# Performance work log

Hardware: AMD Instinct MI355X
Metric: run time of the kernel (lower is better)

## Reference

```python
import jax, jax.numpy as jnp
import numpy as np

N, M, K, D = 65536, 131072, 8, 64
TAU = 0.3
EPS = 1e-6

def setup_inputs() -> dict:
    key = jax.random.key(0)
    ks = jax.random.split(key, 16)
    s = 0.05
    return {
        "f_pts": jax.random.normal(ks[0], (N, D), jnp.float32),
        "pts": jax.random.uniform(ks[1], (N, 3), jnp.float32) * 10.0,
        "z_latent": jax.random.normal(ks[2], (M, D), jnp.float32) * 0.1,
        "centers": jax.random.uniform(ks[3], (M, 3), jnp.float32) * 10.0,
        "cand_idx": jax.random.randint(ks[4], (N, K), 0, M),
        "sim_w1": jax.random.normal(ks[5], (2 * D + 3, 64), jnp.float32) * s,
        "sim_b1": jnp.zeros((64,), jnp.float32),
        "sim_w2": jax.random.normal(ks[6], (64, 1), jnp.float32) * s,
        "sim_b2": jnp.zeros((1,), jnp.float32),
        "gate_w1": jax.random.normal(ks[7], (2 * D, D), jnp.float32) * s,
        "gate_b1": jnp.zeros((D,), jnp.float32),
        "gate_w2": jax.random.normal(ks[8], (D, 1), jnp.float32) * s,
        "gate_b2": jnp.zeros((1,), jnp.float32),
        "W_ih": jax.random.normal(ks[9], (3 * D, D), jnp.float32) * s,
        "W_hh": jax.random.normal(ks[10], (3 * D, D), jnp.float32) * s,
        "b_ih": jnp.zeros((3 * D,), jnp.float32),
        "b_hh": jnp.zeros((3 * D,), jnp.float32),
    }

def _forward(f_pts, pts, z_latent, centers, sim_w1, sim_b1, sim_w2, sim_b2,
             gate_w1, gate_b1, gate_w2, gate_b2, W_ih, W_hh, b_ih, b_hh, cand_idx):
    n, k = cand_idx.shape
    m, d = z_latent.shape
    # --- gather voxel latents / centers for each (point, candidate) pair ---
    z_c = z_latent[cand_idx]                         # (N,K,D)
    delta = pts[:, None, :] - centers[cand_idx]      # (N,K,3)
    f_b = jnp.broadcast_to(f_pts[:, None, :], (n, k, d))
    # --- similarity MLP ---
    x = jnp.concatenate([f_b, z_c, delta], axis=-1)  # (N,K,2D+3)
    h = jax.nn.relu(x @ sim_w1 + sim_b1)
    sim = (h @ sim_w2 + sim_b2)[..., 0]              # (N,K)
    # --- low-temperature top-K routing weights over candidates ---
    w = jax.nn.softmax(sim / TAU, axis=-1)           # (N,K)
    # --- scatter weighted point features to voxels ---
    flat_idx = cand_idx.reshape(-1)                  # (N*K,)
    contrib = (w[..., None] * f_pts[:, None, :]).reshape(-1, d)
    msg = jax.ops.segment_sum(contrib, flat_idx, num_segments=m)     # (M,D)
    wsum = jax.ops.segment_sum(w.reshape(-1), flat_idx, num_segments=m)
    msg = msg / (wsum[:, None] + EPS)                # normalized voxel message
    # --- per-voxel gate ---
    g_in = jnp.concatenate([z_latent, msg], axis=-1)
    gate = jax.nn.sigmoid(jax.nn.relu(g_in @ gate_w1 + gate_b1) @ gate_w2 + gate_b2)  # (M,1)
    # --- GRUCell (torch layout: rows ordered r,z,n) ---
    gi = msg @ W_ih.T + b_ih
    gh = z_latent @ W_hh.T + b_hh
    i_r, i_z, i_n = jnp.split(gi, 3, axis=-1)
    h_r, h_z, h_n = jnp.split(gh, 3, axis=-1)
    r = jax.nn.sigmoid(i_r + h_r)
    zg = jax.nn.sigmoid(i_z + h_z)
    nn_ = jnp.tanh(i_n + r * h_n)
    h_new = (1.0 - zg) * nn_ + zg * z_latent
    # gated latent update
    return z_latent + gate * (h_new - z_latent)

def reference(f_pts, pts, z_latent, centers, cand_idx, sim_w1, sim_b1, sim_w2, sim_b2,
              gate_w1, gate_b1, gate_w2, gate_b2, W_ih, W_hh, b_ih, b_hh):
    return _forward(f_pts, pts, z_latent, centers, sim_w1, sim_b1, sim_w2, sim_b2,
                    gate_w1, gate_b1, gate_w2, gate_b2, W_ih, W_hh, b_ih, b_hh, cand_idx)
```

## Files before the change

kernel.cpp:

```cpp
#include <hip/hip_runtime.h>
#include <hip/hip_fp16.h>
#include <math.h>


typedef short bf16x8 __attribute__((ext_vector_type(8)));
typedef unsigned short u16x8 __attribute__((ext_vector_type(8)));
typedef float f32x4 __attribute__((ext_vector_type(4)));
#define MFMA __builtin_amdgcn_mfma_f32_16x16x32_bf16
#define CAP 32

__device__ __forceinline__ short f2bf(float f) {
  unsigned u = __float_as_uint(f);
  unsigned r = (u + 0x7FFFu + ((u >> 16) & 1u)) >> 16;
  return (short)r;
}

__device__ __forceinline__ float bf2f(unsigned short h) {
  return __uint_as_float(((unsigned)h) << 16);
}

__device__ __forceinline__ float sigm(float x) { return 1.0f / (1.0f + __expf(-x)); }

__global__ __launch_bounds__(256) void prep0_kernel(
    const float* __restrict__ sim_w1, const float* __restrict__ gate_w1,
    const float* __restrict__ W_ih, const float* __restrict__ W_hh,
    short* __restrict__ bfF, short* __restrict__ bfZC,
    short* __restrict__ GF, short* __restrict__ WihF, short* __restrict__ WhhF,
    int* __restrict__ cursor, int M)
{
  int tid = blockIdx.x * 256 + threadIdx.x;
  int n4 = M >> 2;
  int stride = gridDim.x * 256;
  int4* cp = (int4*)cursor;
  for (int j = tid; j < n4; j += stride) cp[j] = make_int4(0, 0, 0, 0);

  int w = blockIdx.x * 4 + (threadIdx.x >> 6);
  int lane = threadIdx.x & 63, lr = lane & 15, lg = lane >> 4;
  bf16x8 o;

  if (w < 12) {
    int ct = w / 3, kt = w % 3;
#pragma unroll
    for (int e = 0; e < 8; ++e) {
      int k = kt * 32 + lg * 8 + e;
      float v = 0.0f;
      if (kt < 2) v = sim_w1[k * 64 + ct * 16 + lr];
      else if ((k - 64) < 3) v = sim_w1[(128 + (k - 64)) * 64 + ct * 16 + lr];
      o[e] = f2bf(v);
    }
    *(bf16x8*)&bfF[w * 512 + lane * 8] = o;
  } else if (w < 24) {
    int q = w - 12, ct = q / 3, kt = q % 3;
#pragma unroll
    for (int e = 0; e < 8; ++e) {
      int k = kt * 32 + lg * 8 + e;
      float v = 0.0f;
      if (kt < 2) v = sim_w1[(64 + k) * 64 + ct * 16 + lr];
      else if ((k - 64) < 3) v = sim_w1[(128 + (k - 64)) * 64 + ct * 16 + lr];
      o[e] = f2bf(v);
    }
    *(bf16x8*)&bfZC[q * 512 + lane * 8] = o;
  } else if (w < 40) {
    int q = w - 24, ct = q >> 2, kt = q & 3;
#pragma unroll
    for (int e = 0; e < 8; ++e)
      o[e] = f2bf(gate_w1[(kt * 32 + lg * 8 + e) * 64 + ct * 16 + lr]);
    *(bf16x8*)&GF[q * 512 + lane * 8] = o;
  } else if (w < 64) {
    int q = w - 40, g = q >> 3, ct = (q >> 1) & 3, k2 = q & 1;
    int row = g * 64 + ct * 16 + lr;
#pragma unroll
    for (int e = 0; e < 8; ++e)
      o[e] = f2bf(W_ih[row * 64 + k2 * 32 + lg * 8 + e]);
    *(bf16x8*)&WihF[q * 512 + lane * 8] = o;
  } else if (w < 88) {
    int q = w - 64, g = q >> 3, ct = (q >> 1) & 3, k2 = q & 1;
    int row = g * 64 + ct * 16 + lr;
#pragma unroll
    for (int e = 0; e < 8; ++e)
      o[e] = f2bf(W_hh[row * 64 + k2 * 32 + lg * 8 + e]);
    *(bf16x8*)&WhhF[q * 512 + lane * 8] = o;
  }
}

__global__ __launch_bounds__(256) void prep_kernel(
    const float* __restrict__ z, const float* __restrict__ f,
    const float* __restrict__ pts, const float* __restrict__ centers,
    const float* __restrict__ sim_b1,
    const short* __restrict__ bfF, const short* __restrict__ bfZC,
    unsigned short* __restrict__ zbf, unsigned short* __restrict__ fbf,
    unsigned short* __restrict__ HBp, unsigned short* __restrict__ ZC)
{
  int g = blockIdx.x * 4 + (threadIdx.x >> 6);
  int lane = threadIdx.x & 63;
  int lr = lane & 15, lg = lane >> 4;

  if (g < 4096) {
    int n0 = g * 16;
    bf16x8 bw[12];
#pragma unroll
    for (int i = 0; i < 12; ++i) bw[i] = *(const bf16x8*)&bfF[i * 512 + lane * 8];

    bf16x8 a[3];
#pragma unroll
    for (int kt = 0; kt < 2; ++kt) {
      const float* src = &f[(long)(n0 + lr) * 64 + kt * 32 + lg * 8];
      float4 v0 = *(const float4*)src;
      float4 v1 = *(const float4*)(src + 4);
      bf16x8 t;
      t[0] = f2bf(v0.x); t[1] = f2bf(v0.y); t[2] = f2bf(v0.z); t[3] = f2bf(v0.w);
      t[4] = f2bf(v1.x); t[5] = f2bf(v1.y); t[6] = f2bf(v1.z); t[7] = f2bf(v1.w);
      a[kt] = t;
    }
    {
      bf16x8 t = {0,0,0,0,0,0,0,0};
      if (lg == 0) {
        t[0] = f2bf(pts[(n0 + lr) * 3 + 0]);
        t[1] = f2bf(pts[(n0 + lr) * 3 + 1]);
        t[2] = f2bf(pts[(n0 + lr) * 3 + 2]);
      }
      a[2] = t;
    }
    *(bf16x8*)&fbf[(long)(n0 + lr) * 64 + lg * 8] = a[0];
    *(bf16x8*)&fbf[(long)(n0 + lr) * 64 + 32 + lg * 8] = a[1];

    f32x4 acc[4] = {{0,0,0,0},{0,0,0,0},{0,0,0,0},{0,0,0,0}};
#pragma unroll
    for (int ct = 0; ct < 4; ++ct)
#pragma unroll
      for (int kt = 0; kt < 3; ++kt)
        acc[ct] = MFMA(a[kt], bw[ct * 3 + kt], acc[ct], 0, 0, 0);

#pragma unroll
    for (int ct = 0; ct < 4; ++ct) {
      float b1 = sim_b1[ct * 16 + lr];
#pragma unroll
      for (int e = 0; e < 4; ++e)
        HBp[(long)(n0 + lg * 4 + e) * 64 + ct * 16 + lr] =
            (unsigned short)f2bf(acc[ct][e] + b1);
    }
  } else if (g < 12288) {
    int r0 = (g - 4096) * 16;
    bf16x8 bw[12];
#pragma unroll
    for (int i = 0; i < 12; ++i) bw[i] = *(const bf16x8*)&bfZC[i * 512 + lane * 8];

    bf16x8 a[3];
#pragma unroll
    for (int kt = 0; kt < 2; ++kt) {
      const float* src = &z[(long)(r0 + lr) * 64 + kt * 32 + lg * 8];
      float4 v0 = *(const float4*)src;
      float4 v1 = *(const float4*)(src + 4);
      bf16x8 t;
      t[0] = f2bf(v0.x); t[1] = f2bf(v0.y); t[2] = f2bf(v0.z); t[3] = f2bf(v0.w);
      t[4] = f2bf(v1.x); t[5] = f2bf(v1.y); t[6] = f2bf(v1.z); t[7] = f2bf(v1.w);
      a[kt] = t;
    }
    {
      bf16x8 t = {0,0,0,0,0,0,0,0};
      if (lg == 0) {
        t[0] = f2bf(-centers[(r0 + lr) * 3 + 0]);
        t[1] = f2bf(-centers[(r0 + lr) * 3 + 1]);
        t[2] = f2bf(-centers[(r0 + lr) * 3 + 2]);
      }
      a[2] = t;
    }
    *(bf16x8*)&zbf[(long)(r0 + lr) * 64 + lg * 8] = a[0];
    *(bf16x8*)&zbf[(long)(r0 + lr) * 64 + 32 + lg * 8] = a[1];

    f32x4 acc[4] = {{0,0,0,0},{0,0,0,0},{0,0,0,0},{0,0,0,0}};
#pragma unroll
    for (int ct = 0; ct < 4; ++ct)
#pragma unroll
      for (int kt = 0; kt < 3; ++kt)
        acc[ct] = MFMA(a[kt], bw[ct * 3 + kt], acc[ct], 0, 0, 0);

#pragma unroll
    for (int ct = 0; ct < 4; ++ct)
#pragma unroll
      for (int e = 0; e < 4; ++e)
        ZC[(long)(r0 + lg * 4 + e) * 64 + ct * 16 + lr] =
            (unsigned short)f2bf(acc[ct][e]);
  }
}

__global__ __launch_bounds__(256) void pair_kernel(
    const unsigned short* __restrict__ HBp, const unsigned short* __restrict__ ZC,
    const int* __restrict__ cand_idx, const float* __restrict__ sim_w2,
    int* __restrict__ cursor, unsigned* __restrict__ rec)
{
  int n = (blockIdx.x * 256 + threadIdx.x) >> 6;
  int lane = threadIdx.x & 63;
  int k = lane & 7, cg = lane >> 3;

  int ci = cand_idx[n * 8 + k];

  uint4 zc4 = *(const uint4*)&ZC[(long)ci * 64 + cg * 8];
  uint4 hb4 = *(const uint4*)&HBp[(long)n * 64 + cg * 8];
  float4 w2a = *(const float4*)&sim_w2[cg * 8];
  float4 w2b = *(const float4*)&sim_w2[cg * 8 + 4];

  float s = 0.f;
  {
    unsigned zd[4] = {zc4.x, zc4.y, zc4.z, zc4.w};
    unsigned hd[4] = {hb4.x, hb4.y, hb4.z, hb4.w};
    float w2v[8] = {w2a.x, w2a.y, w2a.z, w2a.w, w2b.x, w2b.y, w2b.z, w2b.w};
#pragma unroll
    for (int d = 0; d < 4; ++d) {
      float zlo = __uint_as_float(zd[d] << 16);
      float zhi = __uint_as_float(zd[d] & 0xffff0000u);
      float hlo = __uint_as_float(hd[d] << 16);
      float hhi = __uint_as_float(hd[d] & 0xffff0000u);
      s = fmaf(fmaxf(hlo + zlo, 0.f), w2v[2 * d], s);
      s = fmaf(fmaxf(hhi + zhi, 0.f), w2v[2 * d + 1], s);
    }
  }

#pragma unroll
  for (int m = 8; m <= 32; m <<= 1) s += __shfl_xor(s, m, 64);

  float mx = s;
#pragma unroll
  for (int m = 1; m <= 4; m <<= 1) mx = fmaxf(mx, __shfl_xor(mx, m, 64));
  float e = __expf((s - mx) * (1.0f / 0.3f));
  float ss = e;
#pragma unroll
  for (int m = 1; m <= 4; m <<= 1) ss += __shfl_xor(ss, m, 64);
  float w = e / ss;

  if (lane < 8) {
    int slot = atomicAdd(&cursor[ci], 1);
    if (slot < CAP) {
      unsigned short wh = __half_as_ushort(__float2half(w));
      rec[(long)ci * CAP + slot] = ((unsigned)n << 16) | (unsigned)wh;
    }
  }
}

__global__ __launch_bounds__(256) void gather_kernel(
    const unsigned* __restrict__ rec, const int* __restrict__ cursor,
    const unsigned short* __restrict__ fbf, unsigned short* __restrict__ msg_bf,
    int mvox)
{
  int tid = blockIdx.x * 256 + threadIdx.x;
  int row = tid >> 2, seg = tid & 3;
  if (row >= mvox) return;

  int cnt = cursor[row];
  cnt = cnt < CAP ? cnt : CAP;
  const unsigned* rp = &rec[(long)row * CAP];

  float acc[16];
#pragma unroll
  for (int j = 0; j < 16; ++j) acc[j] = 0.f;
  float ws = 0.f;

  for (int i0 = 0; i0 < cnt; i0 += 4) {
    uint4 r4 = *(const uint4*)&rp[i0];
    unsigned rr0 = r4.x, rr1 = r4.y, rr2 = r4.z, rr3 = r4.w;
#pragma unroll
    for (int j = 0; j < 4; ++j) {
      unsigned r = j == 0 ? rr0 : j == 1 ? rr1 : j == 2 ? rr2 : rr3;
      if (i0 + j < cnt) {
        float w = __half2float(__ushort_as_half((unsigned short)(r & 0xffffu)));
        int nn = r >> 16;
        ws += w;
        const u16x8* fp = (const u16x8*)&fbf[(long)nn * 64 + seg * 16];
        u16x8 f0 = fp[0], f1 = fp[1];
#pragma unroll
        for (int kk = 0; kk < 8; ++kk) {
          acc[kk]     = fmaf(w, bf2f(f0[kk]), acc[kk]);
          acc[8 + kk] = fmaf(w, bf2f(f1[kk]), acc[8 + kk]);
        }
      }
    }
  }
  float inv = 1.0f / (ws + 1e-6f);
  u16x8 o0, o1;
#pragma unroll
  for (int j = 0; j < 8; ++j) {
    o0[j] = (unsigned short)f2bf(acc[j] * inv);
    o1[j] = (unsigned short)f2bf(acc[8 + j] * inv);
  }
  *(u16x8*)&msg_bf[(long)row * 64 + seg * 16] = o0;
  *(u16x8*)&msg_bf[(long)row * 64 + seg * 16 + 8] = o1;
}

__global__ __launch_bounds__(512)
__attribute__((amdgpu_waves_per_eu(2)))
void stage2(
    const unsigned short* __restrict__ zbf,
    const short* __restrict__ GF, const short* __restrict__ WihF,
    const short* __restrict__ WhhF,
    const float* __restrict__ gate_b1, const float* __restrict__ gate_w2,
    const float* __restrict__ gate_b2,
    const float* __restrict__ b_ih, const float* __restrict__ b_hh,
    const unsigned short* __restrict__ msg_bf,
    float* __restrict__ out)
{
  __shared__ float gb1s[64], gw2s[64], bihs[192], bhhs[192];
  __shared__ float gb2s;

  int t = threadIdx.x;
  if (t < 64) { gb1s[t] = gate_b1[t]; gw2s[t] = gate_w2[t]; }
  if (t < 192) { bihs[t] = b_ih[t]; bhhs[t] = b_hh[t]; }
  if (t == 0) gb2s = gate_b2[0];
  __syncthreads();

  int wid = t >> 6, lane = t & 63;
  int lr = lane & 15, lg = lane >> 4;

  int rowbase = blockIdx.x * 128 + wid * 16;
  long abase = (long)(rowbase + lr) * 64;
  bf16x8 a0 = *(const bf16x8*)&zbf[abase + lg * 8];
  bf16x8 a1 = *(const bf16x8*)&zbf[abase + 32 + lg * 8];
  bf16x8 a2 = *(const bf16x8*)&msg_bf[abase + lg * 8];
  bf16x8 a3 = *(const bf16x8*)&msg_bf[abase + 32 + lg * 8];

  f32x4 usum = {0.f, 0.f, 0.f, 0.f};
#pragma unroll 1
  for (int ct = 0; ct < 4; ++ct) {
    f32x4 au = {0, 0, 0, 0};
    au = MFMA(a0, *(const bf16x8*)&GF[(ct * 4 + 0) * 512 + lane * 8], au, 0, 0, 0);
    au = MFMA(a1, *(const bf16x8*)&GF[(ct * 4 + 1) * 512 + lane * 8], au, 0, 0, 0);
    au = MFMA(a2, *(const bf16x8*)&GF[(ct * 4 + 2) * 512 + lane * 8], au, 0, 0, 0);
    au = MFMA(a3, *(const bf16x8*)&GF[(ct * 4 + 3) * 512 + lane * 8], au, 0, 0, 0);
    int c = ct * 16 + lr;
#pragma unroll
    for (int e = 0; e < 4; ++e)
      usum[e] += fmaxf(au[e] + gb1s[c], 0.0f) * gw2s[c];
  }
#pragma unroll
  for (int m = 1; m <= 8; m <<= 1)
#pragma unroll
    for (int e = 0; e < 4; ++e) {
      float v = usum[e];
      usum[e] = v + __shfl_xor(v, m, 64);
    }
  float gate[4];
#pragma unroll
  for (int e = 0; e < 4; ++e) gate[e] = sigm(usum[e] + gb2s);

#pragma unroll 1
  for (int ct = 0; ct < 4; ++ct) {
    f32x4 air = {0,0,0,0}, aiz = {0,0,0,0}, ain = {0,0,0,0};
    f32x4 ahr = {0,0,0,0}, ahz = {0,0,0,0}, ahn = {0,0,0,0};
#pragma unroll
    for (int k2 = 0; k2 < 2; ++k2) {
      bf16x8 amg = k2 ? a3 : a2;
      bf16x8 az_ = k2 ? a1 : a0;
      int base = ct * 2 + k2;
      air = MFMA(amg, *(const bf16x8*)&WihF[(      base) * 512 + lane * 8], air, 0, 0, 0);
      aiz = MFMA(amg, *(const bf16x8*)&WihF[( 8 +  base) * 512 + lane * 8], aiz, 0, 0, 0);
      ain = MFMA(amg, *(const bf16x8*)&WihF[(16 +  base) * 512 + lane * 8], ain, 0, 0, 0);
      ahr = MFMA(az_, *(const bf16x8*)&WhhF[(      base) * 512 + lane * 8], ahr, 0, 0, 0);
      ahz = MFMA(az_, *(const bf16x8*)&WhhF[( 8 +  base) * 512 + lane * 8], ahz, 0, 0, 0);
      ahn = MFMA(az_, *(const bf16x8*)&WhhF[(16 +  base) * 512 + lane * 8], ahn, 0, 0, 0);
    }
    int c = ct * 16 + lr;
#pragma unroll
    for (int e = 0; e < 4; ++e) {
      float zv = bf2f(zbf[(long)(rowbase + lg * 4 + e) * 64 + c]);
      float rr = sigm(air[e] + bihs[c] + ahr[e] + bhhs[c]);
      float zg = sigm(aiz[e] + bihs[64 + c] + ahz[e] + bhhs[64 + c]);
      float nn = tanhf(ain[e] + bihs[128 + c] + rr * (ahn[e] + bhhs[128 + c]));
      float hnew = (1.0f - zg) * nn + zg * zv;
      out[(long)(rowbase + lg * 4 + e) * 64 + c] = zv + gate[e] * (hnew - zv);
    }
  }
}

extern "C" void kernel_launch(void* const* d_in, const int* in_sizes, int n_in,
                              void* d_out, int out_size, void* d_ws, size_t ws_size,
                              hipStream_t stream) {
  const float* f_pts   = (const float*)d_in[0];
  const float* pts     = (const float*)d_in[1];
  const float* z_lat   = (const float*)d_in[2];
  const float* centers = (const float*)d_in[3];
  const int*   cand    = (const int*)d_in[4];
  const float* sim_w1  = (const float*)d_in[5];
  const float* sim_b1  = (const float*)d_in[6];
  const float* sim_w2  = (const float*)d_in[7];
  const float* gate_w1 = (const float*)d_in[9];
  const float* gate_b1 = (const float*)d_in[10];
  const float* gate_w2 = (const float*)d_in[11];
  const float* gate_b2 = (const float*)d_in[12];
  const float* W_ih    = (const float*)d_in[13];
  const float* W_hh    = (const float*)d_in[14];
  const float* b_ih    = (const float*)d_in[15];
  const float* b_hh    = (const float*)d_in[16];

  int N = in_sizes[0] / 64;
  int M = in_sizes[2] / 64;

  int* cursor = (int*)d_ws;
  unsigned* rec = (unsigned*)(cursor + M);
  unsigned short* msg_bf = (unsigned short*)rec;
  unsigned short* zbf = (unsigned short*)(rec + (size_t)M * CAP);
  unsigned short* fbf = zbf + (size_t)M * 64;
  unsigned short* HBp = fbf + (size_t)N * 64;
  unsigned short* ZC = HBp + (size_t)N * 64;
  short* bfF = (short*)(ZC + (size_t)M * 64);
  short* bfZC = bfF + 12 * 512;
  short* GF = bfZC + 12 * 512;
  short* WihF = GF + 16 * 512;
  short* WhhF = WihF + 24 * 512;

  prep0_kernel<<<32, 256, 0, stream>>>(sim_w1, gate_w1, W_ih, W_hh,
                                       bfF, bfZC, GF, WihF, WhhF, cursor, M);

  prep_kernel<<<3072, 256, 0, stream>>>(z_lat, f_pts, pts, centers, sim_b1,
                                        bfF, bfZC, zbf, fbf, HBp, ZC);

  pair_kernel<<<N / 4, 256, 0, stream>>>(HBp, ZC, cand, sim_w2, cursor, rec);

  gather_kernel<<<(M * 4) / 256, 256, 0, stream>>>(rec, cursor, fbf, msg_bf, M);

  stage2<<<M / 128, 512, 0, stream>>>(zbf, GF, WihF, WhhF,
                                      gate_b1, gate_w2, gate_b2, b_ih, b_hh,
                                      msg_bf, (float*)d_out);
}
```

Measured before the change: 102.4 us.

## Process eight points per wave in pair_kernel with batched loads and full-lane atomics

Each wave in pair_kernel now handles eight points instead of one. It loads all 64 candidate indices with one coalesced read and broadcasts them with shuffles, then issues all the gathered ZC and HBp loads up front to get more memory requests in flight. The per-point reductions run in a loop, and each lane keeps the softmax weight for its own (point, candidate) pair, so all 64 lanes do the cursor atomic and record write instead of only 8. The grid becomes eight times smaller and register use per thread goes up, which may reduce occupancy.

New measurement: 106.4 us. 1.04x slower.

```diff
diff --git a/kernel.cpp b/kernel.cpp
--- a/kernel.cpp
+++ b/kernel.cpp
@@ -184,27 +184,38 @@
   }
 }
 
+#define PPW 8
 __global__ __launch_bounds__(256) void pair_kernel(
     const unsigned short* __restrict__ HBp, const unsigned short* __restrict__ ZC,
     const int* __restrict__ cand_idx, const float* __restrict__ sim_w2,
     int* __restrict__ cursor, unsigned* __restrict__ rec)
 {
-  int n = (blockIdx.x * 256 + threadIdx.x) >> 6;
+  int wave = (blockIdx.x * 256 + threadIdx.x) >> 6;
   int lane = threadIdx.x & 63;
   int k = lane & 7, cg = lane >> 3;
-
-  int ci = cand_idx[n * 8 + k];
-
-  uint4 zc4 = *(const uint4*)&ZC[(long)ci * 64 + cg * 8];
-  uint4 hb4 = *(const uint4*)&HBp[(long)n * 64 + cg * 8];
+  int n0 = wave * PPW;
+
+  int cl = cand_idx[n0 * 8 + lane];
+
   float4 w2a = *(const float4*)&sim_w2[cg * 8];
   float4 w2b = *(const float4*)&sim_w2[cg * 8 + 4];
-
-  float s = 0.f;
-  {
-    unsigned zd[4] = {zc4.x, zc4.y, zc4.z, zc4.w};
-    unsigned hd[4] = {hb4.x, hb4.y, hb4.z, hb4.w};
-    float w2v[8] = {w2a.x, w2a.y, w2a.z, w2a.w, w2b.x, w2b.y, w2b.z, w2b.w};
+  float w2v[8] = {w2a.x, w2a.y, w2a.z, w2a.w, w2b.x, w2b.y, w2b.z, w2b.w};
+
+  int ci[PPW];
+  uint4 zc[PPW], hb[PPW];
+#pragma unroll
+  for (int p = 0; p < PPW; ++p) {
+    ci[p] = __shfl(cl, p * 8 + k, 64);
+    zc[p] = *(const uint4*)&ZC[(long)ci[p] * 64 + cg * 8];
+    hb[p] = *(const uint4*)&HBp[(long)(n0 + p) * 64 + cg * 8];
+  }
+
+  float myw = 0.f;
+#pragma unroll
+  for (int p = 0; p < PPW; ++p) {
+    unsigned zd[4] = {zc[p].x, zc[p].y, zc[p].z, zc[p].w};
+    unsigned hd[4] = {hb[p].x, hb[p].y, hb[p].z, hb[p].w};
+    float s = 0.f;
 #pragma unroll
     for (int d = 0; d < 4; ++d) {
       float zlo = __uint_as_float(zd[d] << 16);
@@ -214,26 +225,24 @@
       s = fmaf(fmaxf(hlo + zlo, 0.f), w2v[2 * d], s);
       s = fmaf(fmaxf(hhi + zhi, 0.f), w2v[2 * d + 1], s);
     }
-  }
-
-#pragma unroll
-  for (int m = 8; m <= 32; m <<= 1) s += __shfl_xor(s, m, 64);
-
-  float mx = s;
-#pragma unroll
-  for (int m = 1; m <= 4; m <<= 1) mx = fmaxf(mx, __shfl_xor(mx, m, 64));
-  float e = __expf((s - mx) * (1.0f / 0.3f));
-  float ss = e;
-#pragma unroll
-  for (int m = 1; m <= 4; m <<= 1) ss += __shfl_xor(ss, m, 64);
-  float w = e / ss;
-
-  if (lane < 8) {
-    int slot = atomicAdd(&cursor[ci], 1);
-    if (slot < CAP) {
-      unsigned short wh = __half_as_ushort(__float2half(w));
-      rec[(long)ci * CAP + slot] = ((unsigned)n << 16) | (unsigned)wh;
-    }
+#pragma unroll
+    for (int m = 8; m <= 32; m <<= 1) s += __shfl_xor(s, m, 64);
+    float mx = s;
+#pragma unroll
+    for (int m = 1; m <= 4; m <<= 1) mx = fmaxf(mx, __shfl_xor(mx, m, 64));
+    float e = __expf((s - mx) * (1.0f / 0.3f));
+    float ss = e;
+#pragma unroll
+    for (int m = 1; m <= 4; m <<= 1) ss += __shfl_xor(ss, m, 64);
+    float w = e / ss;
+    if (cg == p) myw = w;
+  }
+
+  int slot = atomicAdd(&cursor[cl], 1);
+  if (slot < CAP) {
+    int n_pt = n0 + cg;
+    unsigned short wh = __half_as_ushort(__float2half(myw));
+    rec[(long)cl * CAP + slot] = ((unsigned)n_pt << 16) | (unsigned)wh;
   }
 }
 
@@ -412,7 +421,8 @@
   prep_kernel<<<3072, 256, 0, stream>>>(z_lat, f_pts, pts, centers, sim_b1,
                                         bfF, bfZC, zbf, fbf, HBp, ZC);
 
-  pair_kernel<<<N / 4, 256, 0, stream>>>(HBp, ZC, cand, sim_w2, cursor, rec);
+  pair_kernel<<<N / (4 * PPW), 256, 0, stream>>>(HBp, ZC, cand, sim_w2,
+                                                 cursor, rec);
 
   gather_kernel<<<(M * 4) / 256, 256, 0, stream>>>(rec, cursor, fbf, msg_bf, M);
 
```
